# Kernel optimization log

Measured on AMD Instinct MI355X. Metric: run time of the kernel, lower is better.

Reference implementation:

```python
import jax, jax.numpy as jnp
import numpy as np

B, T, N, H = 16, 12, 1000, 128
NL = 2  # num_layers
EPS = 1e-5


def setup_inputs() -> dict:
    key = jax.random.key(0)
    ks = jax.random.split(key, 16)
    rn = lambda k, s, sc=0.05: jax.random.normal(k, s, jnp.float32) * sc
    return {
        "inputs": jax.random.normal(ks[0], (B, T, N), jnp.float32),
        "adj": jax.random.uniform(ks[1], (N, N), dtype=jnp.float32),
        # per-layer graph-conv params (stacked over NL layers)
        "gc1_w": rn(ks[2], (NL, H + 1, 2 * H)),
        "gc1_b": jnp.ones((NL, 2 * H), jnp.float32),   # bias=1.0 in torch init
        "gc2_w": rn(ks[3], (NL, H + 1, H)),
        "gc2_b": jnp.zeros((NL, H), jnp.float32),
        "ln_g": jnp.ones((NL, H), jnp.float32),
        "ln_b": jnp.zeros((NL, H), jnp.float32),
        "res_w": rn(ks[4], (H,)),   # Linear(1,H) weight squeezed
        "res_b": rn(ks[5], (H,)),
        # GRU tail (unidirectional, 1 layer)
        "gru_wih": rn(ks[6], (3 * H, H)),
        "gru_whh": rn(ks[7], (3 * H, H)),
        "gru_bih": rn(ks[8], (3 * H,)),
        "gru_bhh": rn(ks[9], (3 * H,)),
        "proj_w": rn(ks[10], (H, H)),
        "proj_b": rn(ks[11], (H,)),
        # output MLP
        "out_w1": rn(ks[12], (256, H)),
        "out_b1": rn(ks[13], (256,)),
        "out_w2": rn(ks[14], (H, 256)),
        "out_b2": rn(ks[15], (H,)),
    }


def _laplacian(adj):
    a = jax.nn.softmax(adj, axis=-1)
    m = a + jnp.eye(N, dtype=adj.dtype)           # A + I
    d = m.sum(axis=1)
    dis = jnp.where(d > 0, d ** -0.5, 0.0)
    # matrix.matmul(D^-1/2).T.matmul(D^-1/2)
    return (m * dis[None, :]).T * dis[None, :]


def _gconv(L, x, h, w, b):
    # x: [B,N], h: [B,N,H], concat: [B,N,H+1]
    concat = jnp.concatenate([x[..., None], h], axis=2)
    ac = jnp.einsum("mn,bnk->bmk", L, concat)     # Laplacian graph conv
    return ac @ w + b                              # [B,N,out_dim]


def _cell(L, x, h, w1, b1, w2, b2):
    gates = jax.nn.sigmoid(_gconv(L, x, h, w1, b1))       # [B,N,2H]
    # torch chunks the FLAT [B, N*2H] tensor: split is across nodes!
    flat = gates.reshape(gates.shape[0], N * 2 * H)
    r = flat[:, : N * H].reshape(-1, N, H)
    u = flat[:, N * H :].reshape(-1, N, H)
    c = jnp.tanh(_gconv(L, x, r * h, w2, b2))
    return u * h + (1.0 - u) * c


def _layernorm(x, g, b):
    mu = x.mean(-1, keepdims=True)
    var = jnp.mean((x - mu) ** 2, axis=-1, keepdims=True)
    return (x - mu) * jax.lax.rsqrt(var + EPS) * g + b


def _gru_last(xs, h0, wih, whh, bih, bhh):
    # xs: [T, BN, H]
    def step(h, x):
        gi = x @ wih.T + bih
        gh = h @ whh.T + bhh
        ir, iz, inn = jnp.split(gi, 3, axis=-1)
        hr, hz, hn = jnp.split(gh, 3, axis=-1)
        r = jax.nn.sigmoid(ir + hr)
        z = jax.nn.sigmoid(iz + hz)
        n = jnp.tanh(inn + r * hn)
        return (1.0 - z) * n + z * h, None
    h_last, _ = jax.lax.scan(step, h0, xs)
    return h_last


def reference(inputs, adj, gc1_w, gc1_b, gc2_w, gc2_b, ln_g, ln_b, res_w, res_b,
              gru_wih, gru_whh, gru_bih, gru_bhh, proj_w, proj_b,
              out_w1, out_b1, out_w2, out_b2):
    L = _laplacian(adj)

    def step(hs, x_t):
        x = x_t
        residual = x_t
        new_hs = []
        out = None
        for i in range(NL):
            h = _cell(L, x, hs[i], gc1_w[i], gc1_b[i], gc2_w[i], gc2_b[i])
            new_hs.append(h)
            res = residual[..., None] * res_w + res_b   # Linear(1,H)
            out = _layernorm(h + res, ln_g[i], ln_b[i])  # dropout = identity (eval)
            x = out.mean(axis=2)
            residual = x
        return tuple(new_hs), out

    h0 = tuple(jnp.zeros((B, N, H), jnp.float32) for _ in range(NL))
    xs = jnp.swapaxes(inputs, 0, 1)                 # [T,B,N]
    _, outs = jax.lax.scan(step, h0, xs)            # [T,B,N,H]

    # GRU tail over time, batched across B*N node-sequences
    rnn_xs = jnp.transpose(outs, (0, 1, 2, 3)).reshape(T, B * N, H)
    h_last = _gru_last(rnn_xs, jnp.zeros((B * N, H), jnp.float32),
                       gru_wih, gru_whh, gru_bih, gru_bhh)
    last = h_last @ proj_w.T + proj_b
    o = last.reshape(B, N, H)
    o = jax.nn.relu(o @ out_w1.T + out_b1) @ out_w2.T + out_b2
    return o
```

## Files before the change

kernel.cpp:

```cpp
#include <hip/hip_runtime.h>
#include <math.h>

#define BB 16
#define TT 12
#define NN 1000
#define HH 128
#define CC 129
#define NROW 16000
#define GR 160
#define KP 1024
#define CP2 160
#define SPS 168

#define BUFSZ    22528
#define OFF_SGT  10752
#define OFF_SO   31232
#define OFF_SHB  39936
#define OFF_SCAL 67584
#define OFF_SST  70144
#define SMEMB    72192

typedef __attribute__((ext_vector_type(4))) float f32x4;
typedef __attribute__((ext_vector_type(8))) __bf16 bf16x8;

#define MFMA16(A, B, C) __builtin_amdgcn_mfma_f32_16x16x32_bf16((A), (B), (C), 0, 0, 0)

__device__ __forceinline__ float sigmoidf_(float x) { return 1.0f / (1.0f + expf(-x)); }

__global__ void k_softmax(const float* __restrict__ adj, float* __restrict__ a) {
    int i = blockIdx.x;
    int t = threadIdx.x;
    __shared__ float red[256];
    float m = -1e30f;
    for (int j = t; j < NN; j += 256) m = fmaxf(m, adj[i * NN + j]);
    red[t] = m; __syncthreads();
    for (int s = 128; s > 0; s >>= 1) { if (t < s) red[t] = fmaxf(red[t], red[t + s]); __syncthreads(); }
    m = red[0]; __syncthreads();
    float sum = 0.f;
    for (int j = t; j < NN; j += 256) sum += expf(adj[i * NN + j] - m);
    red[t] = sum; __syncthreads();
    for (int s = 128; s > 0; s >>= 1) { if (t < s) red[t] += red[t + s]; __syncthreads(); }
    float inv = 1.0f / red[0];
    for (int j = t; j < NN; j += 256) a[i * NN + j] = expf(adj[i * NN + j] - m) * inv;
}

__global__ __launch_bounds__(256) void k_build_Lt(const float* __restrict__ a, __bf16* __restrict__ Lb) {
    __shared__ float s[64][65];
    int bi = blockIdx.x * 64;
    int bj = blockIdx.y * 64;
    int t = threadIdx.x;
    for (int q = t; q < 64 * 64; q += 256) {
        int r = q >> 6, c = q & 63;
        int jj = bj + r, ii = bi + c;
        s[r][c] = (jj < NN && ii < NN) ? a[jj * NN + ii] : 0.f;
    }
    __syncthreads();
    for (int q = t; q < 64 * 64; q += 256) {
        int r = q >> 6, c = q & 63;
        int ii = bi + r, jj = bj + c;
        if (ii < NN && jj < NN)
            Lb[(size_t)ii * KP + jj] = (__bf16)(0.5f * (s[c][r] + (ii == jj ? 1.0f : 0.0f)));
    }
}

__global__ void k_prep(const float* __restrict__ wih, const float* __restrict__ whh,
                       const float* __restrict__ proj_w, const float* __restrict__ ow1,
                       const float* __restrict__ ow2, const float* __restrict__ gc1_w,
                       const float* __restrict__ gc2_w,
                       __bf16* __restrict__ WihB, __bf16* __restrict__ WhhB,
                       __bf16* __restrict__ projB, __bf16* __restrict__ w1B,
                       __bf16* __restrict__ w2B, __bf16* __restrict__ W1t,
                       __bf16* __restrict__ W2t) {
    int idx = blockIdx.x * 256 + threadIdx.x;
    if (idx < 49152) { WihB[idx] = (__bf16)wih[idx]; return; }
    idx -= 49152;
    if (idx < 49152) { WhhB[idx] = (__bf16)whh[idx]; return; }
    idx -= 49152;
    if (idx < 16384) { projB[idx] = (__bf16)proj_w[idx]; return; }
    idx -= 16384;
    if (idx < 32768) { w1B[idx] = (__bf16)ow1[idx]; return; }
    idx -= 32768;
    if (idx < 32768) { w2B[idx] = (__bf16)ow2[idx]; return; }
    idx -= 32768;
    if (idx < 2 * 256 * CP2) {
        int l = idx / (256 * CP2); int r = idx % (256 * CP2); int o = r / CP2, c = r % CP2;
        W1t[idx] = (c < CC) ? (__bf16)gc1_w[((size_t)l * CC + c) * 256 + o] : (__bf16)0.f;
        return;
    }
    idx -= 2 * 256 * CP2;
    if (idx < 2 * 128 * CP2) {
        int l = idx / (128 * CP2); int r = idx % (128 * CP2); int o = r / CP2, c = r % CP2;
        W2t[idx] = (c < CC) ? (__bf16)gc2_w[((size_t)l * CC + c) * 128 + o] : (__bf16)0.f;
    }
}

__global__ void k_prep_x(const float* __restrict__ inp, __bf16* __restrict__ G0) {
    int idx = blockIdx.x * 256 + threadIdx.x;
    if (idx >= BB * 1024) return;
    int b = idx >> 10, k = idx & 1023;
    G0[(size_t)b * GR * KP + k] = (k < NN) ? (__bf16)inp[(size_t)b * TT * NN + k] : (__bf16)0.f;
}

#define GL16(SRC, DSTOFF)                                                            \
    __builtin_amdgcn_global_load_lds(                                                \
        (const __attribute__((address_space(1))) unsigned int*)(SRC),                \
        (__attribute__((address_space(3))) unsigned int*)(smem + (DSTOFF)), 16, 0, 0)

template<int MODE, int STORE>
__global__ __launch_bounds__(512) void k_fused(
    const __bf16* __restrict__ Lb, const __bf16* __restrict__ Gf,
    const __bf16* __restrict__ Wt, const float* __restrict__ bias,
    __bf16* __restrict__ GB, __bf16* __restrict__ u, __bf16* __restrict__ h,
    const float* __restrict__ x_in, int xstride,
    const float* __restrict__ res_w, const float* __restrict__ res_b,
    const float* __restrict__ ln_g, const float* __restrict__ ln_b,
    float* __restrict__ x_out, __bf16* __restrict__ Gnext,
    __bf16* __restrict__ GhSelf,
    __bf16* __restrict__ Hb,
    const __bf16* __restrict__ WihB, const __bf16* __restrict__ WhhB,
    const float* __restrict__ bih, const float* __restrict__ bhh,
    const float* __restrict__ inp, __bf16* __restrict__ xnextG, int tnext)
{
    __shared__ __align__(16) char smem[SMEMB];
    __bf16* sP   = (__bf16*)smem;
    __bf16* sGT  = (__bf16*)(smem + OFF_SGT);
    __bf16* sT   = (__bf16*)(smem + OFF_SGT);
    __bf16* sO   = (__bf16*)(smem + OFF_SO);
    float*  sScal= (float*)(smem + OFF_SCAL);
    float*  sSt  = (float*)(smem + OFF_SST);

    int tid = threadIdx.x;
    int wg = blockIdx.x;
    int b = wg & 15;
    int m0 = (wg >> 4) * 32;
    int wave = tid >> 6, lane = tid & 63;
    int lr = lane & 15, lk = lane >> 4;
    int wm = wave >> 2;
    int wcg = wave & 3;
    int cgbase = (wcg == 0) ? 0 : (wcg * 2 + 1) * 16;
    int NC = (wcg == 0) ? 3 : 2;

    if (MODE == 0) {
        if (tid < 256) sScal[tid] = bias[tid];
    } else if (tid < 128) {
        sScal[tid] = bias[tid];
        sScal[128 + tid] = res_w[tid];
        sScal[256 + tid] = res_b[tid];
        sScal[384 + tid] = ln_g[tid];
        sScal[512 + tid] = ln_b[tid];
    }

    size_t srowOff = (size_t)b * GR * KP;
    int rIn = lane >> 3;
    int cswz = ((lane & 7) ^ rIn) * 8;

    int nld = (wave < 6) ? 3 : 2;
    const __bf16* psrc[3];
    int pdst[3];
#pragma unroll
    for (int q = 0; q < 3; q++) {
        int c = wave + q * 8;
        if (c < 22) {
            psrc[q] = (c < 4)
                ? Lb + (size_t)(m0 + c * 8 + rIn) * KP + cswz
                : Gf + srowOff + (size_t)((c - 4) * 8 + rIn) * KP + cswz;
            pdst[q] = c * 1024;
        } else { psrc[q] = nullptr; pdst[q] = 0; }
    }

#define STAGE(BUF, IT) {                                                     \
    _Pragma("unroll")                                                        \
    for (int q = 0; q < 3; q++)                                              \
        if (wave + q * 8 < 22)                                               \
            GL16(psrc[q] + (IT) * 64, (BUF) * BUFSZ + pdst[q]); }

    f32x4 acc[3];
#pragma unroll
    for (int j = 0; j < 3; j++) acc[j] = (f32x4){0.f, 0.f, 0.f, 0.f};

    STAGE(0, 0);
    __syncthreads();
    STAGE(1, 1);
    int bc = 0;
    for (int it = 0; it < 16; ++it) {
        if (it == 15) asm volatile("s_waitcnt vmcnt(0)" ::: "memory");
        else if (nld == 3) asm volatile("s_waitcnt vmcnt(3)" ::: "memory");
        else               asm volatile("s_waitcnt vmcnt(2)" ::: "memory");
        __builtin_amdgcn_s_barrier();
        __builtin_amdgcn_sched_barrier(0);
        const char* bp = smem + bc * BUFSZ;
#pragma unroll
        for (int ks = 0; ks < 2; ks++) {
            int kb = (ks * 64 + lk * 16) ^ ((lr & 7) << 4);
            int chA = wm * 2 + (lr >> 3);
            bf16x8 af = *(const bf16x8*)(bp + chA * 1024 + (lr & 7) * 128 + kb);
#pragma unroll
            for (int cf = 0; cf < 3; cf++) {
                if (cf < NC) {
                    int chB = 4 + (cgbase >> 3) + cf * 2 + (lr >> 3);
                    bf16x8 bfr = *(const bf16x8*)(bp + chB * 1024 + (lr & 7) * 128 + kb);
                    acc[cf] = MFMA16(af, bfr, acc[cf]);
                }
            }
        }
        if (it < 14) { int bs = (it + 2) % 3; STAGE(bs, it + 2); }
        bc = (bc == 2) ? 0 : bc + 1;
    }
    __syncthreads();
#undef STAGE

#pragma unroll
    for (int cf = 0; cf < 3; cf++) {
        if (cf < NC) {
#pragma unroll
            for (int i = 0; i < 4; i++)
                sP[(wm * 16 + lk * 4 + i) * SPS + cgbase + cf * 16 + lr] = (__bf16)acc[cf][i];
        }
    }
    for (int q = tid; q < 32 * 16; q += 512) sP[(q >> 4) * SPS + 144 + (q & 15)] = (__bf16)0.f;
    __syncthreads();

    constexpr int NOF = (MODE == 0) ? 2 : 1;
    int o0 = wave * NOF * 16;
    int j = o0 + lr;
    f32x4 accs[2][NOF];
#pragma unroll
    for (int i = 0; i < 2; i++)
#pragma unroll
        for (int jj = 0; jj < NOF; jj++) accs[i][jj] = (f32x4){0.f, 0.f, 0.f, 0.f};
#pragma unroll
    for (int kk2 = 0; kk2 < CP2; kk2 += 32) {
        bf16x8 pa[2];
#pragma unroll
        for (int mf2 = 0; mf2 < 2; mf2++)
            pa[mf2] = *(const bf16x8*)&sP[(mf2 * 16 + lr) * SPS + kk2 + lk * 8];
#pragma unroll
        for (int of = 0; of < NOF; of++) {
            bf16x8 wb = *(const bf16x8*)&Wt[(size_t)(o0 + of * 16 + lr) * CP2 + kk2 + lk * 8];
#pragma unroll
            for (int mf2 = 0; mf2 < 2; mf2++)
                accs[mf2][of] = MFMA16(pa[mf2], wb, accs[mf2][of]);
        }
    }

    if (MODE == 0) {
        if (tid < 4)
            *(bf16x8*)&GB[srowOff + m0 + tid * 8] = *(const bf16x8*)&Gf[srowOff + m0 + tid * 8];
        bool clean = (m0 + 32 <= 500);
        if (clean) {
#pragma unroll
            for (int of = 0; of < NOF; of++) {
                int o = o0 + of * 16 + lr;
                float bv = sScal[o];
#pragma unroll
                for (int mf2 = 0; mf2 < 2; mf2++)
#pragma unroll
                    for (int i = 0; i < 4; i++)
                        sGT[o * 40 + mf2 * 16 + lk * 4 + i] = (__bf16)sigmoidf_(accs[mf2][of][i] + bv);
            }
            __syncthreads();
            for (int q = tid; q < 128 * 8; q += 512) {
                int jj = q >> 3;
                int rnc = (q & 7) * 4;
                size_t gidx = srowOff + (size_t)(1 + jj) * KP + 2 * m0 + rnc * 2;
                bf16x8 hv = *(const bf16x8*)&Gf[gidx];
                bf16x8 rv;
#pragma unroll
                for (int e = 0; e < 8; e++) {
                    int rnl = rnc + (e >> 1);
                    int hi = e & 1;
                    float g = (float)sGT[(hi * 128 + jj) * 40 + rnl];
                    rv[e] = (__bf16)(g * (float)hv[e]);
                }
                *(bf16x8*)&GB[gidx] = rv;
            }
        } else {
#pragma unroll
            for (int of = 0; of < NOF; of++) {
                int o = o0 + of * 16 + lr;
                int jo = o & 127, hi = o >> 7;
                float bv = sScal[o];
#pragma unroll
                for (int mf2 = 0; mf2 < 2; mf2++)
#pragma unroll
                    for (int i = 0; i < 4; i++) {
                        int m = m0 + mf2 * 16 + lk * 4 + i;
                        if (m >= NN) continue;
                        float g = sigmoidf_(accs[mf2][of][i] + bv);
                        if (m < 500) {
                            size_t gi = srowOff + (size_t)(1 + jo) * KP + 2 * m + hi;
                            GB[gi] = (__bf16)(g * (float)Gf[gi]);
                        } else {
                            u[((size_t)b * NN + 2 * (m - 500) + hi) * HH + jo] = (__bf16)g;
                        }
                    }
            }
        }
    } else {
        float hnv[2][4];
        float mu_[2][4], rs_[2][4];
        float xs_[2][4];
        {
            float s_[2][4], ss_[2][4];
#pragma unroll
            for (int a = 0; a < 2; a++)
#pragma unroll
                for (int i = 0; i < 4; i++) { s_[a][i] = 0.f; ss_[a][i] = 0.f; }
            float b2v = sScal[j], rwv = sScal[128 + j], rbv = sScal[256 + j];
#pragma unroll
            for (int mf2 = 0; mf2 < 2; mf2++) {
#pragma unroll
                for (int i = 0; i < 4; i++) {
                    int m = m0 + mf2 * 16 + lk * 4 + i;
                    int msafe = (m < NN) ? m : (NN - 1);
                    size_t ri = ((size_t)b * NN + msafe) * HH + j;
                    float cv = tanhf(accs[mf2][0][i] + b2v);
                    float uu = (float)u[ri];
                    float hv = (float)h[ri];
                    float hn = uu * hv + (1.f - uu) * cv;
                    if (m < NN) h[ri] = (__bf16)hn;
                    hnv[mf2][i] = hn;
                    float xv = (m < NN) ? x_in[(size_t)b * xstride + m] : 0.f;
                    float y = hn + xv * rwv + rbv;
                    accs[mf2][0][i] = y;
                    s_[mf2][i] += y; ss_[mf2][i] += y * y;
                }
            }
#pragma unroll
            for (int msk = 1; msk < 16; msk <<= 1)
#pragma unroll
                for (int a = 0; a < 2; a++)
#pragma unroll
                    for (int i = 0; i < 4; i++) {
                        s_[a][i] += __shfl_xor(s_[a][i], msk);
                        ss_[a][i] += __shfl_xor(ss_[a][i], msk);
                    }
            if (lr == 0) {
#pragma unroll
                for (int a = 0; a < 2; a++)
#pragma unroll
                    for (int i = 0; i < 4; i++) {
                        int ml = a * 16 + lk * 4 + i;
                        sSt[wave * 32 + ml] = s_[a][i];
                        sSt[256 + wave * 32 + ml] = ss_[a][i];
                    }
            }
        }
        __syncthreads();
        {
#pragma unroll
            for (int a = 0; a < 2; a++)
#pragma unroll
                for (int i = 0; i < 4; i++) {
                    int ml = a * 16 + lk * 4 + i;
                    float S = 0.f, SS = 0.f;
#pragma unroll
                    for (int w = 0; w < 8; w++) { S += sSt[w * 32 + ml]; SS += sSt[256 + w * 32 + ml]; }
                    float mu = S * (1.f / 128.f);
                    float var = SS * (1.f / 128.f) - mu * mu;
                    mu_[a][i] = mu;
                    rs_[a][i] = rsqrtf(var + 1e-5f);
                }
            float lg = sScal[384 + j], lb2 = sScal[512 + j];
#pragma unroll
            for (int mf2 = 0; mf2 < 2; mf2++)
#pragma unroll
                for (int i = 0; i < 4; i++) {
                    float ov = (accs[mf2][0][i] - mu_[mf2][i]) * rs_[mf2][i] * lg + lb2;
                    accs[mf2][0][i] = ov;
                    xs_[mf2][i] = ov;
                }
#pragma unroll
            for (int msk = 1; msk < 16; msk <<= 1)
#pragma unroll
                for (int a = 0; a < 2; a++)
#pragma unroll
                    for (int i = 0; i < 4; i++) xs_[a][i] += __shfl_xor(xs_[a][i], msk);
        }
        __syncthreads();
        if (lr == 0) {
#pragma unroll
            for (int a = 0; a < 2; a++)
#pragma unroll
                for (int i = 0; i < 4; i++)
                    sSt[wave * 32 + a * 16 + lk * 4 + i] = xs_[a][i];
        }
        __syncthreads();
        if (wave == 0 && lr == 0) {
#pragma unroll
            for (int a = 0; a < 2; a++)
#pragma unroll
                for (int i = 0; i < 4; i++) {
                    int ml = a * 16 + lk * 4 + i;
                    int m = m0 + ml;
                    if (m < NN) {
                        float S = 0.f;
#pragma unroll
                        for (int w = 0; w < 8; w++) S += sSt[w * 32 + ml];
                        float xv = S * (1.f / 128.f);
                        if (x_out) x_out[(size_t)b * NN + m] = xv;
                        if (Gnext) Gnext[(size_t)b * GR * KP + m] = (__bf16)xv;
                    }
                }
        }
        {
#pragma unroll
            for (int mf2 = 0; mf2 < 2; mf2++)
#pragma unroll
                for (int i = 0; i < 4; i++)
                    sT[j * 40 + mf2 * 16 + lk * 4 + i] = (__bf16)hnv[mf2][i];
            if (STORE) {
#pragma unroll
                for (int mf2 = 0; mf2 < 2; mf2++)
#pragma unroll
                    for (int i = 0; i < 4; i++)
                        sO[(mf2 * 16 + lk * 4 + i) * 136 + j] = (__bf16)accs[mf2][0][i];
            }
        }
        if (STORE) {
            int row = tid >> 4, c8 = (tid & 15) * 8;
            int m = m0 + row;
            size_t hrow = (size_t)b * NN + ((m < NN) ? m : (NN - 1));
            *(bf16x8*)(smem + OFF_SHB + (row * 136 + c8) * 2) =
                *(const bf16x8*)&Hb[hrow * HH + c8];
        }
        __syncthreads();
        {
            int q = tid;
            int jj = q >> 2, mc = (q & 3) * 8;
            if (m0 + mc < NN)
                *(bf16x8*)&GhSelf[srowOff + (size_t)(1 + jj) * KP + m0 + mc] =
                    *(const bf16x8*)&sT[jj * 40 + mc];
        }
        if (STORE) {
            {
                float br  = bih[j] + bhh[j];
                float bz  = bih[128 + j] + bhh[128 + j];
                float bni = bih[256 + j], bnh = bhh[256 + j];
                const __bf16* wir = WihB + (size_t)j * HH;
                const __bf16* whr = WhhB + (size_t)j * HH;
                const __bf16* wiz = WihB + (size_t)(128 + j) * HH;
                const __bf16* whz = WhhB + (size_t)(128 + j) * HH;
                const __bf16* win = WihB + (size_t)(256 + j) * HH;
                const __bf16* whn = WhhB + (size_t)(256 + j) * HH;
#pragma unroll
                for (int mf = 0; mf < 2; mf++) {
                    f32x4 gr = (f32x4){0.f,0.f,0.f,0.f}, gz = gr, gni = gr, gnh = gr;
#pragma unroll
                    for (int kk = 0; kk < 128; kk += 32) {
                        bf16x8 xa = *(const bf16x8*)&sO[(mf * 16 + lr) * 136 + kk + lk * 8];
                        bf16x8 ha = *(const bf16x8*)(smem + OFF_SHB + ((mf * 16 + lr) * 136 + kk + lk * 8) * 2);
                        gr  = MFMA16(xa, *(const bf16x8*)(wir + kk + lk * 8), gr);
                        gr  = MFMA16(ha, *(const bf16x8*)(whr + kk + lk * 8), gr);
                        gz  = MFMA16(xa, *(const bf16x8*)(wiz + kk + lk * 8), gz);
                        gz  = MFMA16(ha, *(const bf16x8*)(whz + kk + lk * 8), gz);
                        gni = MFMA16(xa, *(const bf16x8*)(win + kk + lk * 8), gni);
                        gnh = MFMA16(ha, *(const bf16x8*)(whn + kk + lk * 8), gnh);
                    }
#pragma unroll
                    for (int i = 0; i < 4; i++) {
                        int m = m0 + mf * 16 + lk * 4 + i;
                        if (m >= NN) continue;
                        size_t ri = ((size_t)b * NN + m) * HH + j;
                        float hv = (float)*(const __bf16*)(smem + OFF_SHB +
                                      ((mf * 16 + lk * 4 + i) * 136 + j) * 2);
                        float rg = sigmoidf_(gr[i] + br);
                        float zg = sigmoidf_(gz[i] + bz);
                        float ng = tanhf(gni[i] + bni + rg * (gnh[i] + bnh));
                        float hp = (1.f - zg) * ng + zg * hv;
                        Hb[ri] = (__bf16)hp;
                    }
                }
            }
            if (tid < 32 && tnext < TT) {
                int n = m0 + tid;
                if (n < NN)
                    xnextG[srowOff + n] = (__bf16)inp[(size_t)b * TT * NN + tnext * NN + n];
            }
        }
    }
}
#undef GL16

__global__ __launch_bounds__(256) void k_head_mfma(const __bf16* __restrict__ Hb,
                                                   const __bf16* __restrict__ projB,
                                                   const float* __restrict__ pb,
                                                   const __bf16* __restrict__ w1B,
                                                   const float* __restrict__ b1,
                                                   const __bf16* __restrict__ w2B,
                                                   const float* __restrict__ b2,
                                                   float* __restrict__ out) {
    __shared__ __align__(16) __bf16 sH1[64 * 136];
    __shared__ __align__(16) __bf16 sH2[64 * 264];
    int tid = threadIdx.x;
    int r0 = blockIdx.x * 64;
    int wv = tid >> 6, lane = tid & 63;
    int lr = lane & 15, lk = lane >> 4;
    int arow = r0 + wv * 16 + lr;

    f32x4 a1[8];
#pragma unroll
    for (int i = 0; i < 8; i++) a1[i] = (f32x4){0.f, 0.f, 0.f, 0.f};
#pragma unroll
    for (int kk = 0; kk < 128; kk += 32) {
        bf16x8 xa = *(const bf16x8*)&Hb[(size_t)arow * HH + kk + lk * 8];
#pragma unroll
        for (int f = 0; f < 8; f++) {
            bf16x8 wb = *(const bf16x8*)&projB[(size_t)(f * 16 + lr) * HH + kk + lk * 8];
            a1[f] = MFMA16(xa, wb, a1[f]);
        }
    }
#pragma unroll
    for (int f = 0; f < 8; f++) {
        int j = f * 16 + lr;
        float bv = pb[j];
#pragma unroll
        for (int i = 0; i < 4; i++)
            sH1[(wv * 16 + lk * 4 + i) * 136 + j] = (__bf16)(a1[f][i] + bv);
    }
    __syncthreads();

    f32x4 a2[16];
#pragma unroll
    for (int i = 0; i < 16; i++) a2[i] = (f32x4){0.f, 0.f, 0.f, 0.f};
#pragma unroll
    for (int kk = 0; kk < 128; kk += 32) {
        bf16x8 pa = *(const bf16x8*)&sH1[(wv * 16 + lr) * 136 + kk + lk * 8];
#pragma unroll
        for (int f = 0; f < 16; f++) {
            bf16x8 wb = *(const bf16x8*)&w1B[(size_t)(f * 16 + lr) * HH + kk + lk * 8];
            a2[f] = MFMA16(pa, wb, a2[f]);
        }
    }
    __syncthreads();
#pragma unroll
    for (int f = 0; f < 16; f++) {
        int o = f * 16 + lr;
        float bv = b1[o];
#pragma unroll
        for (int i = 0; i < 4; i++)
            sH2[(wv * 16 + lk * 4 + i) * 264 + o] = (__bf16)fmaxf(a2[f][i] + bv, 0.f);
    }
    __syncthreads();

    f32x4 a3[8];
#pragma unroll
    for (int i = 0; i < 8; i++) a3[i] = (f32x4){0.f, 0.f, 0.f, 0.f};
#pragma unroll
    for (int kk = 0; kk < 256; kk += 32) {
        bf16x8 pa = *(const bf16x8*)&sH2[(wv * 16 + lr) * 264 + kk + lk * 8];
#pragma unroll
        for (int f = 0; f < 8; f++) {
            bf16x8 wb = *(const bf16x8*)&w2B[(size_t)(f * 16 + lr) * 256 + kk + lk * 8];
            a3[f] = MFMA16(pa, wb, a3[f]);
        }
    }
#pragma unroll
    for (int f = 0; f < 8; f++) {
        int j = f * 16 + lr;
        float bv = b2[j];
#pragma unroll
        for (int i = 0; i < 4; i++)
            out[(size_t)(r0 + wv * 16 + lk * 4 + i) * HH + j] = a3[f][i] + bv;
    }
}

extern "C" void kernel_launch(void* const* d_in, const int* in_sizes, int n_in,
                              void* d_out, int out_size, void* d_ws, size_t ws_size,
                              hipStream_t stream) {
    const float* inp    = (const float*)d_in[0];
    const float* adj    = (const float*)d_in[1];
    const float* gc1_w  = (const float*)d_in[2];
    const float* gc1_b  = (const float*)d_in[3];
    const float* gc2_w  = (const float*)d_in[4];
    const float* gc2_b  = (const float*)d_in[5];
    const float* ln_g   = (const float*)d_in[6];
    const float* ln_b   = (const float*)d_in[7];
    const float* res_w  = (const float*)d_in[8];
    const float* res_b  = (const float*)d_in[9];
    const float* wih    = (const float*)d_in[10];
    const float* whh    = (const float*)d_in[11];
    const float* bih    = (const float*)d_in[12];
    const float* bhh    = (const float*)d_in[13];
    const float* proj_w = (const float*)d_in[14];
    const float* proj_b = (const float*)d_in[15];
    const float* ow1    = (const float*)d_in[16];
    const float* ob1    = (const float*)d_in[17];
    const float* ow2    = (const float*)d_in[18];
    const float* ob2    = (const float*)d_in[19];
    float* out = (float*)d_out;

    char* ws = (char*)d_ws;
    size_t off = 0;
    __bf16* Lb     = (__bf16*)(ws + off); off += (size_t)KP * KP * 2;
    __bf16* Gfull0 = (__bf16*)(ws + off); off += (size_t)BB * GR * KP * 2;
    __bf16* Gfull1 = (__bf16*)(ws + off); off += (size_t)BB * GR * KP * 2;
    __bf16* GfullB = (__bf16*)(ws + off); off += (size_t)BB * GR * KP * 2;
    size_t zgrp1 = off;
    __bf16* h0  = (__bf16*)(ws + off); off += (size_t)NROW * HH * 2;
    __bf16* h1  = (__bf16*)(ws + off); off += (size_t)NROW * HH * 2;
    __bf16* Hb  = (__bf16*)(ws + off); off += (size_t)NROW * HH * 2;
    size_t zgrp2 = off;
    __bf16* u   = (__bf16*)(ws + off); off += (size_t)NROW * HH * 2;
    float* xB   = (float*)(ws + off);  off += NROW * 4;
    __bf16* W1t = (__bf16*)(ws + off); off += (size_t)2 * 256 * CP2 * 2;
    __bf16* W2t = (__bf16*)(ws + off); off += (size_t)2 * 128 * CP2 * 2;
    __bf16* WihB= (__bf16*)(ws + off); off += 49152 * 2;
    __bf16* WhhB= (__bf16*)(ws + off); off += 49152 * 2;
    __bf16* projB=(__bf16*)(ws + off); off += 16384 * 2;
    __bf16* w1B = (__bf16*)(ws + off); off += 32768 * 2;
    __bf16* w2B = (__bf16*)(ws + off); off += 32768 * 2;
    float* a_sm = (float*)u;

    hipMemsetAsync(Lb, 0, zgrp1, stream);
    hipMemsetAsync(h0, 0, zgrp2 - zgrp1, stream);

    k_softmax<<<NN, 256, 0, stream>>>(adj, a_sm);
    k_build_Lt<<<dim3(16, 16), 256, 0, stream>>>(a_sm, Lb);
    k_prep<<<1184, 256, 0, stream>>>(wih, whh, proj_w, ow1, ow2, gc1_w, gc2_w,
                                     WihB, WhhB, projB, w1B, w2B, W1t, W2t);
    k_prep_x<<<64, 256, 0, stream>>>(inp, Gfull0);

    for (int t = 0; t < TT; t++) {
        const float* xs0 = inp + (size_t)t * NN;
        k_fused<0, 0><<<512, 512, 0, stream>>>(Lb, Gfull0, W1t, gc1_b, GfullB, u,
            nullptr, nullptr, 0, nullptr, nullptr, nullptr, nullptr,
            nullptr, nullptr, nullptr,
            nullptr, nullptr, nullptr, nullptr, nullptr, nullptr, nullptr, 0);
        k_fused<1, 0><<<512, 512, 0, stream>>>(Lb, GfullB, W2t, gc2_b, nullptr, u, h0,
            xs0, TT * NN, res_w, res_b, ln_g, ln_b,
            xB, Gfull1, Gfull0,
            nullptr, nullptr, nullptr, nullptr, nullptr, nullptr, nullptr, 0);
        k_fused<0, 0><<<512, 512, 0, stream>>>(Lb, Gfull1, W1t + 256 * CP2, gc1_b + 256, GfullB, u,
            nullptr, nullptr, 0, nullptr, nullptr, nullptr, nullptr,
            nullptr, nullptr, nullptr,
            nullptr, nullptr, nullptr, nullptr, nullptr, nullptr, nullptr, 0);
        k_fused<1, 1><<<512, 512, 0, stream>>>(Lb, GfullB, W2t + 128 * CP2, gc2_b + 128, nullptr, u, h1,
            xB, NN, res_w, res_b, ln_g + 128, ln_b + 128,
            nullptr, nullptr, Gfull1,
            Hb, WihB, WhhB, bih, bhh, inp, Gfull0, t + 1);
    }
    k_head_mfma<<<250, 256, 0, stream>>>(Hb, projB, proj_b, w1B, ob1, w2B, ob2, out);
}
```

Measured before the change: 1.320 ms.

## Fuse per-timestep phases into one kernel with per-batch grid barriers

Each timestep's four graph-conv phase kernels are merged into a single kernel launch. The phases are separated by atomic-counter barriers that each cover only the 32 workgroups serving one batch index. This removes most launch gaps and lets different batches move to the next phase independently, without a device-wide drain. It relies on all 512 workgroups being resident at once, otherwise the spin barriers deadlock. It also adds spin-wait and fence overhead at every phase boundary.

Result: slower. 5.024 ms (+280.5%).

```diff
diff --git a/kernel.cpp b/kernel.cpp
--- a/kernel.cpp
+++ b/kernel.cpp
@@ -26,6 +26,17 @@
 #define MFMA16(A, B, C) __builtin_amdgcn_mfma_f32_16x16x32_bf16((A), (B), (C), 0, 0, 0)
 
 __device__ __forceinline__ float sigmoidf_(float x) { return 1.0f / (1.0f + expf(-x)); }
+
+__device__ __forceinline__ void bbar(int* bar, int idx) {
+    __syncthreads();
+    if (threadIdx.x == 0) {
+        __threadfence();
+        __hip_atomic_fetch_add(bar + idx, 1, __ATOMIC_ACQ_REL, __HIP_MEMORY_SCOPE_AGENT);
+        while (__hip_atomic_load(bar + idx, __ATOMIC_ACQUIRE, __HIP_MEMORY_SCOPE_AGENT) < 32)
+            __builtin_amdgcn_s_sleep(4);
+    }
+    __syncthreads();
+}
 
 __global__ void k_softmax(const float* __restrict__ adj, float* __restrict__ a) {
     int i = blockIdx.x;
@@ -107,7 +118,8 @@
         (__attribute__((address_space(3))) unsigned int*)(smem + (DSTOFF)), 16, 0, 0)
 
 template<int MODE, int STORE>
-__global__ __launch_bounds__(512) void k_fused(
+__device__ __forceinline__ void phase_body(
+    char* smem, int wg, int tid,
     const __bf16* __restrict__ Lb, const __bf16* __restrict__ Gf,
     const __bf16* __restrict__ Wt, const float* __restrict__ bias,
     __bf16* __restrict__ GB, __bf16* __restrict__ u, __bf16* __restrict__ h,
@@ -121,7 +133,6 @@
     const float* __restrict__ bih, const float* __restrict__ bhh,
     const float* __restrict__ inp, __bf16* __restrict__ xnextG, int tnext)
 {
-    __shared__ __align__(16) char smem[SMEMB];
     __bf16* sP   = (__bf16*)smem;
     __bf16* sGT  = (__bf16*)(smem + OFF_SGT);
     __bf16* sT   = (__bf16*)(smem + OFF_SGT);
@@ -129,8 +140,6 @@
     float*  sScal= (float*)(smem + OFF_SCAL);
     float*  sSt  = (float*)(smem + OFF_SST);
 
-    int tid = threadIdx.x;
-    int wg = blockIdx.x;
     int b = wg & 15;
     int m0 = (wg >> 4) * 32;
     int wave = tid >> 6, lane = tid & 63;
@@ -481,6 +490,47 @@
     }
 }
 #undef GL16
+
+__global__ __launch_bounds__(512, 4) void k_step(
+    const __bf16* __restrict__ Lb,
+    __bf16* __restrict__ Gfull0, __bf16* __restrict__ Gfull1, __bf16* __restrict__ GfullB,
+    const __bf16* __restrict__ W1t, const __bf16* __restrict__ W2t,
+    const float* __restrict__ gc1_b, const float* __restrict__ gc2_b,
+    __bf16* __restrict__ u, __bf16* __restrict__ h0, __bf16* __restrict__ h1,
+    const float* __restrict__ inp, float* __restrict__ xB,
+    const float* __restrict__ res_w, const float* __restrict__ res_b,
+    const float* __restrict__ ln_g, const float* __restrict__ ln_b,
+    __bf16* __restrict__ Hb,
+    const __bf16* __restrict__ WihB, const __bf16* __restrict__ WhhB,
+    const float* __restrict__ bih, const float* __restrict__ bhh,
+    int* __restrict__ bar, int t)
+{
+    __shared__ __align__(16) char smem[SMEMB];
+    int wg = blockIdx.x, tid = threadIdx.x;
+    int b = wg & 15;
+    const float* xs0 = inp + (size_t)t * NN;
+    int bbase = t * 48 + b;
+
+    phase_body<0, 0>(smem, wg, tid, Lb, Gfull0, W1t, gc1_b, GfullB, u,
+                     nullptr, nullptr, 0, nullptr, nullptr, nullptr, nullptr,
+                     nullptr, nullptr, nullptr, nullptr, nullptr, nullptr,
+                     nullptr, nullptr, nullptr, nullptr, 0);
+    bbar(bar, bbase);
+    phase_body<1, 0>(smem, wg, tid, Lb, GfullB, W2t, gc2_b, nullptr, u, h0,
+                     xs0, TT * NN, res_w, res_b, ln_g, ln_b,
+                     xB, Gfull1, Gfull0, nullptr, nullptr, nullptr, nullptr, nullptr,
+                     nullptr, nullptr, 0);
+    bbar(bar, bbase + 16);
+    phase_body<0, 0>(smem, wg, tid, Lb, Gfull1, W1t + 256 * CP2, gc1_b + 256, GfullB, u,
+                     nullptr, nullptr, 0, nullptr, nullptr, nullptr, nullptr,
+                     nullptr, nullptr, nullptr, nullptr, nullptr, nullptr,
+                     nullptr, nullptr, nullptr, nullptr, 0);
+    bbar(bar, bbase + 32);
+    phase_body<1, 1>(smem, wg, tid, Lb, GfullB, W2t + 128 * CP2, gc2_b + 128, nullptr, u, h1,
+                     xB, NN, res_w, res_b, ln_g + 128, ln_b + 128,
+                     nullptr, nullptr, Gfull1, Hb, WihB, WhhB, bih, bhh,
+                     inp, Gfull0, t + 1);
+}
 
 __global__ __launch_bounds__(256) void k_head_mfma(const __bf16* __restrict__ Hb,
                                                    const __bf16* __restrict__ projB,
@@ -610,10 +660,12 @@
     __bf16* projB=(__bf16*)(ws + off); off += 16384 * 2;
     __bf16* w1B = (__bf16*)(ws + off); off += 32768 * 2;
     __bf16* w2B = (__bf16*)(ws + off); off += 32768 * 2;
+    int* bar    = (int*)(ws + off);    off += 1024 * sizeof(int);
     float* a_sm = (float*)u;
 
     hipMemsetAsync(Lb, 0, zgrp1, stream);
     hipMemsetAsync(h0, 0, zgrp2 - zgrp1, stream);
+    hipMemsetAsync(bar, 0, 1024 * sizeof(int), stream);
 
     k_softmax<<<NN, 256, 0, stream>>>(adj, a_sm);
     k_build_Lt<<<dim3(16, 16), 256, 0, stream>>>(a_sm, Lb);
@@ -622,23 +674,10 @@
     k_prep_x<<<64, 256, 0, stream>>>(inp, Gfull0);
 
     for (int t = 0; t < TT; t++) {
-        const float* xs0 = inp + (size_t)t * NN;
-        k_fused<0, 0><<<512, 512, 0, stream>>>(Lb, Gfull0, W1t, gc1_b, GfullB, u,
-            nullptr, nullptr, 0, nullptr, nullptr, nullptr, nullptr,
-            nullptr, nullptr, nullptr,
-            nullptr, nullptr, nullptr, nullptr, nullptr, nullptr, nullptr, 0);
-        k_fused<1, 0><<<512, 512, 0, stream>>>(Lb, GfullB, W2t, gc2_b, nullptr, u, h0,
-            xs0, TT * NN, res_w, res_b, ln_g, ln_b,
-            xB, Gfull1, Gfull0,
-            nullptr, nullptr, nullptr, nullptr, nullptr, nullptr, nullptr, 0);
-        k_fused<0, 0><<<512, 512, 0, stream>>>(Lb, Gfull1, W1t + 256 * CP2, gc1_b + 256, GfullB, u,
-            nullptr, nullptr, 0, nullptr, nullptr, nullptr, nullptr,
-            nullptr, nullptr, nullptr,
-            nullptr, nullptr, nullptr, nullptr, nullptr, nullptr, nullptr, 0);
-        k_fused<1, 1><<<512, 512, 0, stream>>>(Lb, GfullB, W2t + 128 * CP2, gc2_b + 128, nullptr, u, h1,
-            xB, NN, res_w, res_b, ln_g + 128, ln_b + 128,
-            nullptr, nullptr, Gfull1,
-            Hb, WihB, WhhB, bih, bhh, inp, Gfull0, t + 1);
+        k_step<<<512, 512, 0, stream>>>(Lb, Gfull0, Gfull1, GfullB, W1t, W2t,
+                                        gc1_b, gc2_b, u, h0, h1, inp, xB,
+                                        res_w, res_b, ln_g, ln_b,
+                                        Hb, WihB, WhhB, bih, bhh, bar, t);
     }
     k_head_mfma<<<250, 256, 0, stream>>>(Hb, projB, proj_b, w1B, ob1, w2B, ob2, out);
 }
```

## Software-pipeline layer 1 of step t+1 with layer 2 of step t in dual-phase kernels

Applied to the files above, without the earlier changes.

Layer-0 work for timestep t+1 now runs in the same launch as layer-1 work for timestep t. Each phase is wrapped in a device function driven by a parameter struct, and a k_dual kernel launches 1024 blocks that split between the two phases. Intermediate buffers (GfB, u, xB) are double-buffered to remove the conflicts this creates. The goal is to halve the number of serialized launches and fill the GPU with twice as many workgroups per launch. In exchange, it adds runtime branches on struct fields and more register and shared-memory pressure, and correctness depends on the cross-step data dependencies being exactly right.

Result: slower. 1.360 ms (+3.0%).

```diff
diff --git a/kernel.cpp b/kernel.cpp
--- a/kernel.cpp
+++ b/kernel.cpp
@@ -26,6 +26,16 @@
 #define MFMA16(A, B, C) __builtin_amdgcn_mfma_f32_16x16x32_bf16((A), (B), (C), 0, 0, 0)
 
 __device__ __forceinline__ float sigmoidf_(float x) { return 1.0f / (1.0f + expf(-x)); }
+
+struct PArgs {
+    const __bf16* Gf; const __bf16* Wt; const float* bias;
+    __bf16* GB; __bf16* u; __bf16* h;
+    const float* x_in; int xstride;
+    const float* res_w; const float* res_b; const float* ln_g; const float* ln_b;
+    float* x_out; __bf16* Gnext; __bf16* GhSelf;
+    __bf16* xnextG; int tnext;
+    int store; int active;
+};
 
 __global__ void k_softmax(const float* __restrict__ adj, float* __restrict__ a) {
     int i = blockIdx.x;
@@ -106,22 +116,14 @@
         (const __attribute__((address_space(1))) unsigned int*)(SRC),                \
         (__attribute__((address_space(3))) unsigned int*)(smem + (DSTOFF)), 16, 0, 0)
 
-template<int MODE, int STORE>
-__global__ __launch_bounds__(512) void k_fused(
-    const __bf16* __restrict__ Lb, const __bf16* __restrict__ Gf,
-    const __bf16* __restrict__ Wt, const float* __restrict__ bias,
-    __bf16* __restrict__ GB, __bf16* __restrict__ u, __bf16* __restrict__ h,
-    const float* __restrict__ x_in, int xstride,
-    const float* __restrict__ res_w, const float* __restrict__ res_b,
-    const float* __restrict__ ln_g, const float* __restrict__ ln_b,
-    float* __restrict__ x_out, __bf16* __restrict__ Gnext,
-    __bf16* __restrict__ GhSelf,
-    __bf16* __restrict__ Hb,
+template<int MODE>
+__device__ __forceinline__ void phase_body(
+    char* smem, int wg, int tid, const PArgs& a,
+    const __bf16* __restrict__ Lb, __bf16* __restrict__ Hb,
     const __bf16* __restrict__ WihB, const __bf16* __restrict__ WhhB,
     const float* __restrict__ bih, const float* __restrict__ bhh,
-    const float* __restrict__ inp, __bf16* __restrict__ xnextG, int tnext)
+    const float* __restrict__ inp)
 {
-    __shared__ __align__(16) char smem[SMEMB];
     __bf16* sP   = (__bf16*)smem;
     __bf16* sGT  = (__bf16*)(smem + OFF_SGT);
     __bf16* sT   = (__bf16*)(smem + OFF_SGT);
@@ -129,8 +131,6 @@
     float*  sScal= (float*)(smem + OFF_SCAL);
     float*  sSt  = (float*)(smem + OFF_SST);
 
-    int tid = threadIdx.x;
-    int wg = blockIdx.x;
     int b = wg & 15;
     int m0 = (wg >> 4) * 32;
     int wave = tid >> 6, lane = tid & 63;
@@ -141,13 +141,13 @@
     int NC = (wcg == 0) ? 3 : 2;
 
     if (MODE == 0) {
-        if (tid < 256) sScal[tid] = bias[tid];
+        if (tid < 256) sScal[tid] = a.bias[tid];
     } else if (tid < 128) {
-        sScal[tid] = bias[tid];
-        sScal[128 + tid] = res_w[tid];
-        sScal[256 + tid] = res_b[tid];
-        sScal[384 + tid] = ln_g[tid];
-        sScal[512 + tid] = ln_b[tid];
+        sScal[tid] = a.bias[tid];
+        sScal[128 + tid] = a.res_w[tid];
+        sScal[256 + tid] = a.res_b[tid];
+        sScal[384 + tid] = a.ln_g[tid];
+        sScal[512 + tid] = a.ln_b[tid];
     }
 
     size_t srowOff = (size_t)b * GR * KP;
@@ -163,7 +163,7 @@
         if (c < 22) {
             psrc[q] = (c < 4)
                 ? Lb + (size_t)(m0 + c * 8 + rIn) * KP + cswz
-                : Gf + srowOff + (size_t)((c - 4) * 8 + rIn) * KP + cswz;
+                : a.Gf + srowOff + (size_t)((c - 4) * 8 + rIn) * KP + cswz;
             pdst[q] = c * 1024;
         } else { psrc[q] = nullptr; pdst[q] = 0; }
     }
@@ -236,7 +236,7 @@
             pa[mf2] = *(const bf16x8*)&sP[(mf2 * 16 + lr) * SPS + kk2 + lk * 8];
 #pragma unroll
         for (int of = 0; of < NOF; of++) {
-            bf16x8 wb = *(const bf16x8*)&Wt[(size_t)(o0 + of * 16 + lr) * CP2 + kk2 + lk * 8];
+            bf16x8 wb = *(const bf16x8*)&a.Wt[(size_t)(o0 + of * 16 + lr) * CP2 + kk2 + lk * 8];
 #pragma unroll
             for (int mf2 = 0; mf2 < 2; mf2++)
                 accs[mf2][of] = MFMA16(pa[mf2], wb, accs[mf2][of]);
@@ -245,7 +245,7 @@
 
     if (MODE == 0) {
         if (tid < 4)
-            *(bf16x8*)&GB[srowOff + m0 + tid * 8] = *(const bf16x8*)&Gf[srowOff + m0 + tid * 8];
+            *(bf16x8*)&a.GB[srowOff + m0 + tid * 8] = *(const bf16x8*)&a.Gf[srowOff + m0 + tid * 8];
         bool clean = (m0 + 32 <= 500);
         if (clean) {
 #pragma unroll
@@ -263,7 +263,7 @@
                 int jj = q >> 3;
                 int rnc = (q & 7) * 4;
                 size_t gidx = srowOff + (size_t)(1 + jj) * KP + 2 * m0 + rnc * 2;
-                bf16x8 hv = *(const bf16x8*)&Gf[gidx];
+                bf16x8 hv = *(const bf16x8*)&a.Gf[gidx];
                 bf16x8 rv;
 #pragma unroll
                 for (int e = 0; e < 8; e++) {
@@ -272,7 +272,7 @@
                     float g = (float)sGT[(hi * 128 + jj) * 40 + rnl];
                     rv[e] = (__bf16)(g * (float)hv[e]);
                 }
-                *(bf16x8*)&GB[gidx] = rv;
+                *(bf16x8*)&a.GB[gidx] = rv;
             }
         } else {
 #pragma unroll
@@ -289,9 +289,9 @@
                         float g = sigmoidf_(accs[mf2][of][i] + bv);
                         if (m < 500) {
                             size_t gi = srowOff + (size_t)(1 + jo) * KP + 2 * m + hi;
-                            GB[gi] = (__bf16)(g * (float)Gf[gi]);
+                            a.GB[gi] = (__bf16)(g * (float)a.Gf[gi]);
                         } else {
-                            u[((size_t)b * NN + 2 * (m - 500) + hi) * HH + jo] = (__bf16)g;
+                            a.u[((size_t)b * NN + 2 * (m - 500) + hi) * HH + jo] = (__bf16)g;
                         }
                     }
             }
@@ -303,9 +303,9 @@
         {
             float s_[2][4], ss_[2][4];
 #pragma unroll
-            for (int a = 0; a < 2; a++)
-#pragma unroll
-                for (int i = 0; i < 4; i++) { s_[a][i] = 0.f; ss_[a][i] = 0.f; }
+            for (int aa = 0; aa < 2; aa++)
+#pragma unroll
+                for (int i = 0; i < 4; i++) { s_[aa][i] = 0.f; ss_[aa][i] = 0.f; }
             float b2v = sScal[j], rwv = sScal[128 + j], rbv = sScal[256 + j];
 #pragma unroll
             for (int mf2 = 0; mf2 < 2; mf2++) {
@@ -315,12 +315,12 @@
                     int msafe = (m < NN) ? m : (NN - 1);
                     size_t ri = ((size_t)b * NN + msafe) * HH + j;
                     float cv = tanhf(accs[mf2][0][i] + b2v);
-                    float uu = (float)u[ri];
-                    float hv = (float)h[ri];
+                    float uu = (float)a.u[ri];
+                    float hv = (float)a.h[ri];
                     float hn = uu * hv + (1.f - uu) * cv;
-                    if (m < NN) h[ri] = (__bf16)hn;
+                    if (m < NN) a.h[ri] = (__bf16)hn;
                     hnv[mf2][i] = hn;
-                    float xv = (m < NN) ? x_in[(size_t)b * xstride + m] : 0.f;
+                    float xv = (m < NN) ? a.x_in[(size_t)b * a.xstride + m] : 0.f;
                     float y = hn + xv * rwv + rbv;
                     accs[mf2][0][i] = y;
                     s_[mf2][i] += y; ss_[mf2][i] += y * y;
@@ -329,37 +329,37 @@
 #pragma unroll
             for (int msk = 1; msk < 16; msk <<= 1)
 #pragma unroll
-                for (int a = 0; a < 2; a++)
+                for (int aa = 0; aa < 2; aa++)
 #pragma unroll
                     for (int i = 0; i < 4; i++) {
-                        s_[a][i] += __shfl_xor(s_[a][i], msk);
-                        ss_[a][i] += __shfl_xor(ss_[a][i], msk);
+                        s_[aa][i] += __shfl_xor(s_[aa][i], msk);
+                        ss_[aa][i] += __shfl_xor(ss_[aa][i], msk);
                     }
             if (lr == 0) {
 #pragma unroll
-                for (int a = 0; a < 2; a++)
+                for (int aa = 0; aa < 2; aa++)
 #pragma unroll
                     for (int i = 0; i < 4; i++) {
-                        int ml = a * 16 + lk * 4 + i;
-                        sSt[wave * 32 + ml] = s_[a][i];
-                        sSt[256 + wave * 32 + ml] = ss_[a][i];
+                        int ml = aa * 16 + lk * 4 + i;
+                        sSt[wave * 32 + ml] = s_[aa][i];
+                        sSt[256 + wave * 32 + ml] = ss_[aa][i];
                     }
             }
         }
         __syncthreads();
         {
 #pragma unroll
-            for (int a = 0; a < 2; a++)
+            for (int aa = 0; aa < 2; aa++)
 #pragma unroll
                 for (int i = 0; i < 4; i++) {
-                    int ml = a * 16 + lk * 4 + i;
+                    int ml = aa * 16 + lk * 4 + i;
                     float S = 0.f, SS = 0.f;
 #pragma unroll
                     for (int w = 0; w < 8; w++) { S += sSt[w * 32 + ml]; SS += sSt[256 + w * 32 + ml]; }
                     float mu = S * (1.f / 128.f);
                     float var = SS * (1.f / 128.f) - mu * mu;
-                    mu_[a][i] = mu;
-                    rs_[a][i] = rsqrtf(var + 1e-5f);
+                    mu_[aa][i] = mu;
+                    rs_[aa][i] = rsqrtf(var + 1e-5f);
                 }
             float lg = sScal[384 + j], lb2 = sScal[512 + j];
 #pragma unroll
@@ -373,33 +373,33 @@
 #pragma unroll
             for (int msk = 1; msk < 16; msk <<= 1)
 #pragma unroll
-                for (int a = 0; a < 2; a++)
-#pragma unroll
-                    for (int i = 0; i < 4; i++) xs_[a][i] += __shfl_xor(xs_[a][i], msk);
+                for (int aa = 0; aa < 2; aa++)
+#pragma unroll
+                    for (int i = 0; i < 4; i++) xs_[aa][i] += __shfl_xor(xs_[aa][i], msk);
         }
         __syncthreads();
         if (lr == 0) {
 #pragma unroll
-            for (int a = 0; a < 2; a++)
+            for (int aa = 0; aa < 2; aa++)
 #pragma unroll
                 for (int i = 0; i < 4; i++)
-                    sSt[wave * 32 + a * 16 + lk * 4 + i] = xs_[a][i];
+                    sSt[wave * 32 + aa * 16 + lk * 4 + i] = xs_[aa][i];
         }
         __syncthreads();
         if (wave == 0 && lr == 0) {
 #pragma unroll
-            for (int a = 0; a < 2; a++)
+            for (int aa = 0; aa < 2; aa++)
 #pragma unroll
                 for (int i = 0; i < 4; i++) {
-                    int ml = a * 16 + lk * 4 + i;
+                    int ml = aa * 16 + lk * 4 + i;
                     int m = m0 + ml;
                     if (m < NN) {
                         float S = 0.f;
 #pragma unroll
                         for (int w = 0; w < 8; w++) S += sSt[w * 32 + ml];
                         float xv = S * (1.f / 128.f);
-                        if (x_out) x_out[(size_t)b * NN + m] = xv;
-                        if (Gnext) Gnext[(size_t)b * GR * KP + m] = (__bf16)xv;
+                        if (a.x_out) a.x_out[(size_t)b * NN + m] = xv;
+                        if (a.Gnext) a.Gnext[(size_t)b * GR * KP + m] = (__bf16)xv;
                     }
                 }
         }
@@ -409,7 +409,7 @@
 #pragma unroll
                 for (int i = 0; i < 4; i++)
                     sT[j * 40 + mf2 * 16 + lk * 4 + i] = (__bf16)hnv[mf2][i];
-            if (STORE) {
+            if (a.store) {
 #pragma unroll
                 for (int mf2 = 0; mf2 < 2; mf2++)
 #pragma unroll
@@ -417,7 +417,7 @@
                         sO[(mf2 * 16 + lk * 4 + i) * 136 + j] = (__bf16)accs[mf2][0][i];
             }
         }
-        if (STORE) {
+        if (a.store) {
             int row = tid >> 4, c8 = (tid & 15) * 8;
             int m = m0 + row;
             size_t hrow = (size_t)b * NN + ((m < NN) ? m : (NN - 1));
@@ -429,58 +429,71 @@
             int q = tid;
             int jj = q >> 2, mc = (q & 3) * 8;
             if (m0 + mc < NN)
-                *(bf16x8*)&GhSelf[srowOff + (size_t)(1 + jj) * KP + m0 + mc] =
+                *(bf16x8*)&a.GhSelf[srowOff + (size_t)(1 + jj) * KP + m0 + mc] =
                     *(const bf16x8*)&sT[jj * 40 + mc];
         }
-        if (STORE) {
-            {
-                float br  = bih[j] + bhh[j];
-                float bz  = bih[128 + j] + bhh[128 + j];
-                float bni = bih[256 + j], bnh = bhh[256 + j];
-                const __bf16* wir = WihB + (size_t)j * HH;
-                const __bf16* whr = WhhB + (size_t)j * HH;
-                const __bf16* wiz = WihB + (size_t)(128 + j) * HH;
-                const __bf16* whz = WhhB + (size_t)(128 + j) * HH;
-                const __bf16* win = WihB + (size_t)(256 + j) * HH;
-                const __bf16* whn = WhhB + (size_t)(256 + j) * HH;
-#pragma unroll
-                for (int mf = 0; mf < 2; mf++) {
-                    f32x4 gr = (f32x4){0.f,0.f,0.f,0.f}, gz = gr, gni = gr, gnh = gr;
-#pragma unroll
-                    for (int kk = 0; kk < 128; kk += 32) {
-                        bf16x8 xa = *(const bf16x8*)&sO[(mf * 16 + lr) * 136 + kk + lk * 8];
-                        bf16x8 ha = *(const bf16x8*)(smem + OFF_SHB + ((mf * 16 + lr) * 136 + kk + lk * 8) * 2);
-                        gr  = MFMA16(xa, *(const bf16x8*)(wir + kk + lk * 8), gr);
-                        gr  = MFMA16(ha, *(const bf16x8*)(whr + kk + lk * 8), gr);
-                        gz  = MFMA16(xa, *(const bf16x8*)(wiz + kk + lk * 8), gz);
-                        gz  = MFMA16(ha, *(const bf16x8*)(whz + kk + lk * 8), gz);
-                        gni = MFMA16(xa, *(const bf16x8*)(win + kk + lk * 8), gni);
-                        gnh = MFMA16(ha, *(const bf16x8*)(whn + kk + lk * 8), gnh);
-                    }
-#pragma unroll
-                    for (int i = 0; i < 4; i++) {
-                        int m = m0 + mf * 16 + lk * 4 + i;
-                        if (m >= NN) continue;
-                        size_t ri = ((size_t)b * NN + m) * HH + j;
-                        float hv = (float)*(const __bf16*)(smem + OFF_SHB +
-                                      ((mf * 16 + lk * 4 + i) * 136 + j) * 2);
-                        float rg = sigmoidf_(gr[i] + br);
-                        float zg = sigmoidf_(gz[i] + bz);
-                        float ng = tanhf(gni[i] + bni + rg * (gnh[i] + bnh));
-                        float hp = (1.f - zg) * ng + zg * hv;
-                        Hb[ri] = (__bf16)hp;
-                    }
-                }
-            }
-            if (tid < 32 && tnext < TT) {
-                int n = m0 + tid;
-                if (n < NN)
-                    xnextG[srowOff + n] = (__bf16)inp[(size_t)b * TT * NN + tnext * NN + n];
-            }
+        if (a.store) {
+            float br  = bih[j] + bhh[j];
+            float bz  = bih[128 + j] + bhh[128 + j];
+            float bni = bih[256 + j], bnh = bhh[256 + j];
+            const __bf16* wir = WihB + (size_t)j * HH;
+            const __bf16* whr = WhhB + (size_t)j * HH;
+            const __bf16* wiz = WihB + (size_t)(128 + j) * HH;
+            const __bf16* whz = WhhB + (size_t)(128 + j) * HH;
+            const __bf16* win = WihB + (size_t)(256 + j) * HH;
+            const __bf16* whn = WhhB + (size_t)(256 + j) * HH;
+#pragma unroll
+            for (int mf = 0; mf < 2; mf++) {
+                f32x4 gr = (f32x4){0.f,0.f,0.f,0.f}, gz = gr, gni = gr, gnh = gr;
+#pragma unroll
+                for (int kk = 0; kk < 128; kk += 32) {
+                    bf16x8 xa = *(const bf16x8*)&sO[(mf * 16 + lr) * 136 + kk + lk * 8];
+                    bf16x8 ha = *(const bf16x8*)(smem + OFF_SHB + ((mf * 16 + lr) * 136 + kk + lk * 8) * 2);
+                    gr  = MFMA16(xa, *(const bf16x8*)(wir + kk + lk * 8), gr);
+                    gr  = MFMA16(ha, *(const bf16x8*)(whr + kk + lk * 8), gr);
+                    gz  = MFMA16(xa, *(const bf16x8*)(wiz + kk + lk * 8), gz);
+                    gz  = MFMA16(ha, *(const bf16x8*)(whz + kk + lk * 8), gz);
+                    gni = MFMA16(xa, *(const bf16x8*)(win + kk + lk * 8), gni);
+                    gnh = MFMA16(ha, *(const bf16x8*)(whn + kk + lk * 8), gnh);
+                }
+#pragma unroll
+                for (int i = 0; i < 4; i++) {
+                    int m = m0 + mf * 16 + lk * 4 + i;
+                    if (m >= NN) continue;
+                    size_t ri = ((size_t)b * NN + m) * HH + j;
+                    float hv = (float)*(const __bf16*)(smem + OFF_SHB +
+                                  ((mf * 16 + lk * 4 + i) * 136 + j) * 2);
+                    float rg = sigmoidf_(gr[i] + br);
+                    float zg = sigmoidf_(gz[i] + bz);
+                    float ng = tanhf(gni[i] + bni + rg * (gnh[i] + bnh));
+                    float hp = (1.f - zg) * ng + zg * hv;
+                    Hb[ri] = (__bf16)hp;
+                }
+            }
+        }
+        if (a.xnextG && tid < 32 && a.tnext < TT) {
+            int n = m0 + tid;
+            if (n < NN)
+                a.xnextG[srowOff + n] = (__bf16)inp[(size_t)b * TT * NN + a.tnext * NN + n];
         }
     }
 }
 #undef GL16
+
+template<int MODE>
+__global__ __launch_bounds__(512) void k_dual(
+    PArgs a0, PArgs a1,
+    const __bf16* __restrict__ Lb, __bf16* __restrict__ Hb,
+    const __bf16* __restrict__ WihB, const __bf16* __restrict__ WhhB,
+    const float* __restrict__ bih, const float* __restrict__ bhh,
+    const float* __restrict__ inp)
+{
+    __shared__ __align__(16) char smem[SMEMB];
+    int wg = blockIdx.x, tid = threadIdx.x;
+    const PArgs& a = (wg < 512) ? a0 : a1;
+    if (!a.active) return;
+    phase_body<MODE>(smem, wg & 511, tid, a, Lb, Hb, WihB, WhhB, bih, bhh, inp);
+}
 
 __global__ __launch_bounds__(256) void k_head_mfma(const __bf16* __restrict__ Hb,
                                                    const __bf16* __restrict__ projB,
@@ -595,14 +608,17 @@
     __bf16* Lb     = (__bf16*)(ws + off); off += (size_t)KP * KP * 2;
     __bf16* Gfull0 = (__bf16*)(ws + off); off += (size_t)BB * GR * KP * 2;
     __bf16* Gfull1 = (__bf16*)(ws + off); off += (size_t)BB * GR * KP * 2;
-    __bf16* GfullB = (__bf16*)(ws + off); off += (size_t)BB * GR * KP * 2;
+    __bf16* GfB0   = (__bf16*)(ws + off); off += (size_t)BB * GR * KP * 2;
+    __bf16* GfB1   = (__bf16*)(ws + off); off += (size_t)BB * GR * KP * 2;
     size_t zgrp1 = off;
     __bf16* h0  = (__bf16*)(ws + off); off += (size_t)NROW * HH * 2;
     __bf16* h1  = (__bf16*)(ws + off); off += (size_t)NROW * HH * 2;
     __bf16* Hb  = (__bf16*)(ws + off); off += (size_t)NROW * HH * 2;
     size_t zgrp2 = off;
-    __bf16* u   = (__bf16*)(ws + off); off += (size_t)NROW * HH * 2;
-    float* xB   = (float*)(ws + off);  off += NROW * 4;
+    __bf16* u0  = (__bf16*)(ws + off); off += (size_t)NROW * HH * 2;
+    __bf16* u1  = (__bf16*)(ws + off); off += (size_t)NROW * HH * 2;
+    float* xBa  = (float*)(ws + off);  off += NROW * 4;
+    float* xBb  = (float*)(ws + off);  off += NROW * 4;
     __bf16* W1t = (__bf16*)(ws + off); off += (size_t)2 * 256 * CP2 * 2;
     __bf16* W2t = (__bf16*)(ws + off); off += (size_t)2 * 128 * CP2 * 2;
     __bf16* WihB= (__bf16*)(ws + off); off += 49152 * 2;
@@ -610,7 +626,7 @@
     __bf16* projB=(__bf16*)(ws + off); off += 16384 * 2;
     __bf16* w1B = (__bf16*)(ws + off); off += 32768 * 2;
     __bf16* w2B = (__bf16*)(ws + off); off += 32768 * 2;
-    float* a_sm = (float*)u;
+    float* a_sm = (float*)u0;
 
     hipMemsetAsync(Lb, 0, zgrp1, stream);
     hipMemsetAsync(h0, 0, zgrp2 - zgrp1, stream);
@@ -621,24 +637,50 @@
                                      WihB, WhhB, projB, w1B, w2B, W1t, W2t);
     k_prep_x<<<64, 256, 0, stream>>>(inp, Gfull0);
 
+    PArgs inact = {};
+    inact.active = 0;
+
+    auto mkP1 = [&](int t) {
+        PArgs p = {};
+        p.Gf = Gfull0; p.Wt = W1t; p.bias = gc1_b; p.GB = GfB0; p.u = u0;
+        p.active = 1;
+        return p;
+    };
+    auto mkP2 = [&](int t) {
+        PArgs p = {};
+        p.Gf = GfB0; p.Wt = W2t; p.bias = gc2_b; p.u = u0; p.h = h0;
+        p.x_in = inp + (size_t)t * NN; p.xstride = TT * NN;
+        p.res_w = res_w; p.res_b = res_b; p.ln_g = ln_g; p.ln_b = ln_b;
+        p.x_out = (t & 1) ? xBb : xBa;
+        p.Gnext = Gfull1; p.GhSelf = Gfull0;
+        p.xnextG = Gfull0; p.tnext = t + 1;
+        p.store = 0; p.active = 1;
+        return p;
+    };
+    auto mkP3 = [&](int t) {
+        PArgs p = {};
+        p.Gf = Gfull1; p.Wt = W1t + 256 * CP2; p.bias = gc1_b + 256; p.GB = GfB1; p.u = u1;
+        p.active = 1;
+        return p;
+    };
+    auto mkP4 = [&](int t) {
+        PArgs p = {};
+        p.Gf = GfB1; p.Wt = W2t + 128 * CP2; p.bias = gc2_b + 128; p.u = u1; p.h = h1;
+        p.x_in = (t & 1) ? xBb : xBa; p.xstride = NN;
+        p.res_w = res_w; p.res_b = res_b; p.ln_g = ln_g + 128; p.ln_b = ln_b + 128;
+        p.x_out = nullptr; p.Gnext = nullptr; p.GhSelf = Gfull1;
+        p.xnextG = nullptr; p.tnext = 0;
+        p.store = 1; p.active = 1;
+        return p;
+    };
+
+    k_dual<0><<<1024, 512, 0, stream>>>(mkP1(0), inact, Lb, Hb, WihB, WhhB, bih, bhh, inp);
+    k_dual<1><<<1024, 512, 0, stream>>>(mkP2(0), inact, Lb, Hb, WihB, WhhB, bih, bhh, inp);
     for (int t = 0; t < TT; t++) {
-        const float* xs0 = inp + (size_t)t * NN;
-        k_fused<0, 0><<<512, 512, 0, stream>>>(Lb, Gfull0, W1t, gc1_b, GfullB, u,
-            nullptr, nullptr, 0, nullptr, nullptr, nullptr, nullptr,
-            nullptr, nullptr, nullptr,
-            nullptr, nullptr, nullptr, nullptr, nullptr, nullptr, nullptr, 0);
-        k_fused<1, 0><<<512, 512, 0, stream>>>(Lb, GfullB, W2t, gc2_b, nullptr, u, h0,
-            xs0, TT * NN, res_w, res_b, ln_g, ln_b,
-            xB, Gfull1, Gfull0,
-            nullptr, nullptr, nullptr, nullptr, nullptr, nullptr, nullptr, 0);
-        k_fused<0, 0><<<512, 512, 0, stream>>>(Lb, Gfull1, W1t + 256 * CP2, gc1_b + 256, GfullB, u,
-            nullptr, nullptr, 0, nullptr, nullptr, nullptr, nullptr,
-            nullptr, nullptr, nullptr,
-            nullptr, nullptr, nullptr, nullptr, nullptr, nullptr, nullptr, 0);
-        k_fused<1, 1><<<512, 512, 0, stream>>>(Lb, GfullB, W2t + 128 * CP2, gc2_b + 128, nullptr, u, h1,
-            xB, NN, res_w, res_b, ln_g + 128, ln_b + 128,
-            nullptr, nullptr, Gfull1,
-            Hb, WihB, WhhB, bih, bhh, inp, Gfull0, t + 1);
+        PArgs b1a = (t + 1 < TT) ? mkP1(t + 1) : inact;
+        k_dual<0><<<1024, 512, 0, stream>>>(mkP3(t), b1a, Lb, Hb, WihB, WhhB, bih, bhh, inp);
+        PArgs b2a = (t + 1 < TT) ? mkP2(t + 1) : inact;
+        k_dual<1><<<1024, 512, 0, stream>>>(mkP4(t), b2a, Lb, Hb, WihB, WhhB, bih, bhh, inp);
     }
     k_head_mfma<<<250, 256, 0, stream>>>(Hb, projB, proj_b, w1B, ob1, w2B, ob2, out);
 }
```
